# Optimization experiments

Hardware: AMD Instinct MI355X
Metric: run time of the kernel (lower is better)

Reference implementation:

```python
import jax, jax.numpy as jnp
import numpy as np

V = 512      # visible_size (channel_size, reverse_nodes=False)
H = 512      # hidden_size
FULL = V + H # full_size = 1024
T = 128      # timesteps
LAM = 0.5    # params['lambda']


def _build_lambda():
    # Lambda: (V, FULL); first V cols = lambda, hidden cols = 1, diagonal = 1
    Lam = jnp.concatenate([jnp.full((V, V), LAM, jnp.float32),
                           jnp.ones((V, H), jnp.float32)], axis=1)
    idx = jnp.arange(V)
    return Lam.at[idx, idx].set(1.0)


def setup_inputs() -> dict:
    key = jax.random.key(0)
    k1, k2, k3 = jax.random.split(key, 3)
    X = jax.random.normal(k1, (T, V), jnp.float32)
    W = jax.random.normal(k2, (FULL, FULL), jnp.float32) / np.float32(np.sqrt(FULL))
    b = jax.random.normal(k3, (FULL,), jnp.float32) * 0.01
    return {"X": X, "W": W, "b": b}


def reference(X, W, b):
    Lam = _build_lambda()          # (V, FULL)
    one_minus = 1.0 - Lam[:, :V]   # (V, V); zero on diagonal

    def step(carry, x_t):
        R, _ = carry
        WR = R @ W.T + b                           # Linear: (V, FULL)
        U = Lam * WR                               # masked recurrent part
        # Y has x_t broadcast across rows in first V cols, zeros elsewhere
        U = U.at[:, :V].add(one_minus * x_t[None, :])
        return (jax.nn.relu(U), U), None           # R = phi(U)

    init = (jnp.zeros((V, FULL), jnp.float32), jnp.zeros((V, FULL), jnp.float32))
    (_, U_last), _ = jax.lax.scan(step, init, X)
    return jnp.diagonal(U_last[:, :V])             # (V,)
```

## Files before the change

kernel.cpp:

```cpp
#include <hip/hip_runtime.h>
#include <stdint.h>

#define Vv 512
#define Ff 1024

typedef unsigned short u16;
typedef unsigned long long u64;
typedef __attribute__((ext_vector_type(8))) short s16x8;
typedef __attribute__((ext_vector_type(4))) float f32x4;

#define OFF_WH  (0ull)
#define OFF_WM  (2ull << 20)
#define OFF_WL  (4ull << 20)
#define OFF_A0  (6ull << 20)
#define OFF_A1  (9ull << 20)
#define OFF_FLG (12ull << 20)


__device__ __forceinline__ void split3(float v, u16& h, u16& m, u16& l) {
    unsigned u = __float_as_uint(v);
    float fh = __uint_as_float(u & 0xFFFF0000u);
    h = (u16)(u >> 16);
    float r1 = v - fh;
    unsigned u1 = __float_as_uint(r1);
    float fm = __uint_as_float(u1 & 0xFFFF0000u);
    m = (u16)(u1 >> 16);
    float r2 = r1 - fm;
    l = (u16)(__float_as_uint(r2) >> 16);
}

__device__ __forceinline__ float bf2f(short v) {
    return __uint_as_float(((unsigned)(u16)v) << 16);
}

__global__ void wsplit_kernel(const float* __restrict__ W, char* __restrict__ ws) {
    int idx = blockIdx.x * 256 + threadIdx.x;
    int j = idx >> 7, ko = idx & 127;
    const float* wr = W + (size_t)j * Ff + ko * 8;
    s16x8 vh, vm, vl;
#pragma unroll
    for (int e = 0; e < 8; ++e) {
        u16 h, m, l; split3(wr[e], h, m, l);
        vh[e] = (short)h; vm[e] = (short)m; vl[e] = (short)l;
    }
    int js = j >> 6, nq = (j >> 4) & 3, col = j & 15;
    int c = ko >> 3, kh = (ko >> 2) & 1, o = ko & 3;
    unsigned uhm = (unsigned)((((js * 4 + nq) * 16 + c) * 2 + kh) * 64 + o * 16 + col);
    unsigned ul  = (unsigned)(js * 8192 + (c * 2 + kh) * 256 + o * 64 + nq * 16 + col);
    *(s16x8*)(ws + OFF_WH + (size_t)uhm * 16) = vh;
    *(s16x8*)(ws + OFF_WM + (size_t)uhm * 16) = vm;
    *(s16x8*)(ws + OFF_WL + (size_t)ul * 16)  = vl;
}

__global__ void init_kernel(const float* __restrict__ X, const float* __restrict__ b,
                            char* __restrict__ ws) {
    int idx = blockIdx.x * 256 + threadIdx.x;
    if (idx < 256) ((unsigned*)(ws + OFF_FLG))[idx] = 0u;
    int i = idx >> 7, jo = idx & 127;
    s16x8 vh, vm, vl;
#pragma unroll
    for (int e = 0; e < 8; ++e) {
        int j = jo * 8 + e;
        float u = b[j];
        if (j < Vv && i != j) u = 0.5f * u + 0.5f * X[j];
        u = fmaxf(u, 0.f);
        u16 h, m, l; split3(u, h, m, l);
        vh[e] = (short)h; vm[e] = (short)m; vl[e] = (short)l;
    }
    int ig = i >> 5, r = i & 31, js = jo >> 3, o = jo & 7;
    size_t tb = (size_t)(ig * 16 + js) * 12288 + (size_t)(o * 32 + r) * 16;
    *(s16x8*)(ws + OFF_A0 + tb)        = vh;
    *(s16x8*)(ws + OFF_A0 + tb + 4096) = vm;
    *(s16x8*)(ws + OFF_A0 + tb + 8192) = vl;
}

#define GST(addr, val) \
    asm volatile("global_store_dwordx2 %0, %1, off sc0 sc1" \
                 :: "v"((void*)(addr)), "v"(val) : "memory")
#define MM(acc_, a_, b_) \
    asm("v_mfma_f32_16x16x32_bf16 %0, %1, %2, %0" : "+v"(acc_) : "v"(a_), "v"(b_))

__global__ __launch_bounds__(512, 2)
void mega_kernel(const float* __restrict__ X, const float* __restrict__ b,
                 char* __restrict__ ws) {
    extern __shared__ char smem[];
    const int tid = threadIdx.x, bid = blockIdx.x;
    const int ig = bid >> 4, js = bid & 15;
    const int lane = tid & 63, l15 = lane & 15, l4 = lane >> 4;
    const int w = tid >> 6, kh = w & 1, nq = w >> 1;

    unsigned* flg = (unsigned*)(ws + OFF_FLG);

    {
        const char* src = ws + OFF_WL + (size_t)js * 131072;
#pragma unroll
        for (int q = 0; q < 16; ++q) {
            unsigned u = (unsigned)(q * 512 + tid) * 16u;
            __builtin_amdgcn_global_load_lds(
                (const __attribute__((address_space(1))) void*)(src + u),
                (__attribute__((address_space(3))) void*)(smem + u), 16, 0, 0);
        }
    }

    s16x8 Bh0, Bh1, Bh2, Bh3, Bh4, Bh5, Bh6, Bh7, Bh8, Bh9, Bh10, Bh11, Bh12, Bh13, Bh14, Bh15;
    s16x8 Bm0, Bm1, Bm2, Bm3, Bm4, Bm5, Bm6, Bm7, Bm8, Bm9, Bm10, Bm11, Bm12, Bm13, Bm14, Bm15;
    {
        const char* wbase = ws + OFF_WH +
            (size_t)(((((js * 4 + nq) * 16) * 2 + kh) * 64) + l4 * 16 + l15) * 16;
#define LOADW(c) do {                                                                  \
        asm volatile("global_load_dwordx4 %0, %1, off"                                 \
                     : "=v"(Bh##c) : "v"((const void*)(wbase + (c) * 2048)));          \
        asm volatile("global_load_dwordx4 %0, %1, off"                                 \
                     : "=v"(Bm##c) : "v"((const void*)(wbase + (c) * 2048 + (2ull << 20)))); \
    } while (0)
        LOADW(0);  LOADW(1);  LOADW(2);  LOADW(3);
        LOADW(4);  LOADW(5);  LOADW(6);  LOADW(7);
        LOADW(8);  LOADW(9);  LOADW(10); LOADW(11);
        LOADW(12); LOADW(13); LOADW(14); LOADW(15);
#undef LOADW
    }
    asm volatile("s_waitcnt vmcnt(0)" ::: "memory");

    const int row = tid >> 4, c4 = (tid & 15) * 4;
    const int i_glob = ig * 32 + row;
    const float4 bbv = *(const float4*)(b + js * 64 + c4);
    float* red = (float*)(smem + 131072);

    const unsigned abase = (unsigned)(((kh * 4 + l4) * 32 + l15) * 16);
    const unsigned a00 = abase,          a01 = abase + 256;
    const unsigned a10 = abase + 4096,   a11 = abase + 4096 + 256;
    const unsigned a20 = abase + 8192,   a21 = abase + 8192 + 256;
    const unsigned bloff = (unsigned)(kh * 4096 + (l4 * 64 + nq * 16 + l15) * 16);

    __syncthreads();

    s16x8 Af00, Af01, Af10, Af11, Af20, Af21, Bl;
    u64 ga0, ga1, ga2, gb0, gb1, gb2;

#define GLDA3(g0_, g1_, g2_, cc) do {                                                  \
        const char* ap_ = tb + (size_t)((cc) * 12288) + (size_t)tid * 8;               \
        asm volatile("global_load_dwordx2 %0, %1, off sc0 sc1"                         \
                     : "=v"(g0_) : "v"((const void*)ap_) : "memory");                  \
        asm volatile("global_load_dwordx2 %0, %1, off sc0 sc1"                         \
                     : "=v"(g1_) : "v"((const void*)(ap_ + 4096)) : "memory");         \
        asm volatile("global_load_dwordx2 %0, %1, off sc0 sc1"                         \
                     : "=v"(g2_) : "v"((const void*)(ap_ + 8192)) : "memory");         \
    } while (0)
#define DSWR3(slot, g0_, g1_, g2_) do {                                                \
        char* wp_ = smem + 131072 + (slot) * 12288 + (size_t)tid * 8;                  \
        *(u64*)(wp_) = g0_; *(u64*)(wp_ + 4096) = g1_; *(u64*)(wp_ + 8192) = g2_;      \
    } while (0)
#define DSRD7(slot, cc) do {                                                           \
        const char* sb_ = smem + 131072 + (slot) * 12288;                              \
        Af00 = *(const s16x8*)(sb_ + a00); Af01 = *(const s16x8*)(sb_ + a01);          \
        Af10 = *(const s16x8*)(sb_ + a10); Af11 = *(const s16x8*)(sb_ + a11);          \
        Af20 = *(const s16x8*)(sb_ + a20); Af21 = *(const s16x8*)(sb_ + a21);          \
        Bl = *(const s16x8*)(smem + (cc) * 8192 + bloff);                              \
    } while (0)
#define MFMA12(c) do {                                                                 \
        __builtin_amdgcn_s_setprio(1);                                                 \
        MM(acc0, Af00, Bh##c); MM(acc1, Af01, Bh##c);                                  \
        MM(acc0, Af00, Bm##c); MM(acc1, Af01, Bm##c);                                  \
        MM(acc0, Af10, Bh##c); MM(acc1, Af11, Bh##c);                                  \
        MM(acc0, Af00, Bl);    MM(acc1, Af01, Bl);                                     \
        MM(acc0, Af20, Bh##c); MM(acc1, Af21, Bh##c);                                  \
        MM(acc0, Af10, Bm##c); MM(acc1, Af11, Bm##c);                                  \
        __builtin_amdgcn_s_setprio(0);                                                 \
    } while (0)
#define CHUNK_MID(c, P0, P1, P2, Q0, Q1, Q2) do {                                      \
        GLDA3(P0, P1, P2, (c) + 2);                                                    \
        __builtin_amdgcn_sched_barrier(0);                                             \
        MFMA12(c);                                                                     \
        __builtin_amdgcn_sched_barrier(0);                                             \
        asm volatile("s_waitcnt vmcnt(3)" ::: "memory");                               \
        DSWR3(((c) + 1) & 1, Q0, Q1, Q2);                                              \
        asm volatile("s_waitcnt lgkmcnt(0)" ::: "memory");                             \
        __builtin_amdgcn_s_barrier();                                                  \
        DSRD7(((c) + 1) & 1, (c) + 1);                                                 \
    } while (0)

    for (int t = 1; t <= 126; ++t) {
        char* srcA = ws + ((t & 1) ? OFF_A0 : OFF_A1);
        char* dstA = ws + ((t & 1) ? OFF_A1 : OFF_A0);

        if (tid < 16) {
            while ((int)__hip_atomic_load(&flg[ig * 16 + tid], __ATOMIC_RELAXED,
                                          __HIP_MEMORY_SCOPE_AGENT) < t - 1)
                __builtin_amdgcn_s_sleep(1);
        }
        __syncthreads();
        asm volatile("" ::: "memory");

        const char* tb = srcA + (size_t)ig * 16 * 12288;
        GLDA3(ga0, ga1, ga2, 0);
        GLDA3(gb0, gb1, gb2, 1);
        asm volatile("s_waitcnt vmcnt(3)" ::: "memory");
        DSWR3(0, ga0, ga1, ga2);
        asm volatile("s_waitcnt lgkmcnt(0)" ::: "memory");
        __builtin_amdgcn_s_barrier();
        DSRD7(0, 0);

        f32x4 acc0 = (f32x4){0.f, 0.f, 0.f, 0.f};
        f32x4 acc1 = (f32x4){0.f, 0.f, 0.f, 0.f};

        CHUNK_MID(0,  ga0, ga1, ga2, gb0, gb1, gb2);
        CHUNK_MID(1,  gb0, gb1, gb2, ga0, ga1, ga2);
        CHUNK_MID(2,  ga0, ga1, ga2, gb0, gb1, gb2);
        CHUNK_MID(3,  gb0, gb1, gb2, ga0, ga1, ga2);
        CHUNK_MID(4,  ga0, ga1, ga2, gb0, gb1, gb2);
        CHUNK_MID(5,  gb0, gb1, gb2, ga0, ga1, ga2);
        CHUNK_MID(6,  ga0, ga1, ga2, gb0, gb1, gb2);
        CHUNK_MID(7,  gb0, gb1, gb2, ga0, ga1, ga2);
        CHUNK_MID(8,  ga0, ga1, ga2, gb0, gb1, gb2);
        CHUNK_MID(9,  gb0, gb1, gb2, ga0, ga1, ga2);
        CHUNK_MID(10, ga0, ga1, ga2, gb0, gb1, gb2);
        CHUNK_MID(11, gb0, gb1, gb2, ga0, ga1, ga2);
        CHUNK_MID(12, ga0, ga1, ga2, gb0, gb1, gb2);
        CHUNK_MID(13, gb0, gb1, gb2, ga0, ga1, ga2);
        MFMA12(14);
        asm volatile("s_waitcnt vmcnt(0)" ::: "memory");
        DSWR3(1, gb0, gb1, gb2);
        asm volatile("s_waitcnt lgkmcnt(0)" ::: "memory");
        __builtin_amdgcn_s_barrier();
        DSRD7(1, 15);
        MFMA12(15);

        __builtin_amdgcn_s_barrier();
        asm volatile("s_nop 7\n\ts_nop 7");

#pragma unroll
        for (int r = 0; r < 4; ++r)
            red[w * 512 + (l4 * 4 + r) * 16 + l15] = acc0[r];
#pragma unroll
        for (int r = 0; r < 4; ++r)
            red[w * 512 + (16 + l4 * 4 + r) * 16 + l15] = acc1[r];
        __syncthreads();

        {
            const int nqo = c4 >> 4, cl0 = c4 & 15;
            float4 p0 = *(const float4*)&red[(nqo * 2 + 0) * 512 + row * 16 + cl0];
            float4 p1 = *(const float4*)&red[(nqo * 2 + 1) * 512 + row * 16 + cl0];
            float s0 = p0.x + p1.x, s1 = p0.y + p1.y, s2 = p0.z + p1.z, s3 = p0.w + p1.w;
            const float* xt = X + (size_t)t * Vv;
            float u0 = s0 + bbv.x, u1 = s1 + bbv.y, u2 = s2 + bbv.z, u3 = s3 + bbv.w;
            if (js < 8) {
                int j0 = js * 64 + c4;
                float x0 = xt[j0], x1 = xt[j0 + 1], x2 = xt[j0 + 2], x3 = xt[j0 + 3];
                if (i_glob != j0)     u0 = 0.5f * u0 + 0.5f * x0;
                if (i_glob != j0 + 1) u1 = 0.5f * u1 + 0.5f * x1;
                if (i_glob != j0 + 2) u2 = 0.5f * u2 + 0.5f * x2;
                if (i_glob != j0 + 3) u3 = 0.5f * u3 + 0.5f * x3;
            }
            u0 = fmaxf(u0, 0.f); u1 = fmaxf(u1, 0.f);
            u2 = fmaxf(u2, 0.f); u3 = fmaxf(u3, 0.f);
            u16 h0, m0, l0, h1, m1, l1, h2, m2, l2, h3, m3, l3;
            split3(u0, h0, m0, l0); split3(u1, h1, m1, l1);
            split3(u2, h2, m2, l2); split3(u3, h3, m3, l3);
            u64 ph = (u64)h0 | ((u64)h1 << 16) | ((u64)h2 << 32) | ((u64)h3 << 48);
            u64 pm = (u64)m0 | ((u64)m1 << 16) | ((u64)m2 << 32) | ((u64)m3 << 48);
            u64 pl = (u64)l0 | ((u64)l1 << 16) | ((u64)l2 << 32) | ((u64)l3 << 48);
            size_t tbo = (size_t)(ig * 16 + js) * 12288
                       + (size_t)((c4 >> 3) * 32 + row) * 16 + (c4 & 7) * 2;
            GST(dstA + tbo, ph);
            GST(dstA + tbo + 4096, pm);
            GST(dstA + tbo + 8192, pl);
        }
        asm volatile("s_waitcnt vmcnt(0)" ::: "memory");
        __syncthreads();
        if (tid == 0)
            __hip_atomic_store(&flg[ig * 16 + js], (unsigned)t, __ATOMIC_RELAXED,
                               __HIP_MEMORY_SCOPE_AGENT);
    }
#undef GLDA3
#undef DSWR3
#undef DSRD7
#undef MFMA12
#undef CHUNK_MID
}

__global__ void diag_kernel(const char* __restrict__ ws, const float* __restrict__ W,
                            const float* __restrict__ b, float* __restrict__ out) {
    int i = blockIdx.x, lane = threadIdx.x;
    const char* A0 = ws + OFF_A0;
    float s = 0.f;
#pragma unroll
    for (int rep = 0; rep < 2; ++rep) {
        int ko = lane + rep * 64;
        int js = ko >> 3, o = ko & 7;
        size_t tb = (size_t)((i >> 5) * 16 + js) * 12288
                  + (size_t)(o * 32 + (i & 31)) * 16;
        s16x8 vh = *(const s16x8*)(A0 + tb);
        s16x8 vm = *(const s16x8*)(A0 + tb + 4096);
        s16x8 vl = *(const s16x8*)(A0 + tb + 8192);
        const float* wr = W + (size_t)i * Ff + ko * 8;
#pragma unroll
        for (int e = 0; e < 8; ++e)
            s += (bf2f(vh[e]) + bf2f(vm[e]) + bf2f(vl[e])) * wr[e];
    }
#pragma unroll
    for (int off = 32; off > 0; off >>= 1) s += __shfl_down(s, off);
    if (lane == 0) out[i] = s + b[i];
}

extern "C" void kernel_launch(void* const* d_in, const int* in_sizes, int n_in,
                              void* d_out, int out_size, void* d_ws, size_t ws_size,
                              hipStream_t stream) {
    const float* X = (const float*)d_in[0];
    const float* W = (const float*)d_in[1];
    const float* b = (const float*)d_in[2];
    float* out = (float*)d_out;
    char* ws = (char*)d_ws;

    hipFuncSetAttribute(reinterpret_cast<const void*>(mega_kernel),
                        hipFuncAttributeMaxDynamicSharedMemorySize, 155648);

    wsplit_kernel<<<512, 256, 0, stream>>>(W, ws);
    init_kernel<<<256, 256, 0, stream>>>(X, b, ws);
    mega_kernel<<<256, 512, 155648, stream>>>(X, b, ws);
    diag_kernel<<<512, 64, 0, stream>>>(ws, W, b, out);
}
```

Baseline: 1.093 ms.

## Stream W hi/mid fragments per chunk instead of pinning them in registers

```diff
diff --git a/kernel.cpp b/kernel.cpp
--- a/kernel.cpp
+++ b/kernel.cpp
@@ -55,7 +55,7 @@
 __global__ void init_kernel(const float* __restrict__ X, const float* __restrict__ b,
                             char* __restrict__ ws) {
     int idx = blockIdx.x * 256 + threadIdx.x;
-    if (idx < 256) ((unsigned*)(ws + OFF_FLG))[idx] = 0u;
+    if (idx < 4096) ((unsigned*)(ws + OFF_FLG))[idx] = 0u;
     int i = idx >> 7, jo = idx & 127;
     s16x8 vh, vm, vl;
 #pragma unroll
@@ -102,24 +102,8 @@
         }
     }
 
-    s16x8 Bh0, Bh1, Bh2, Bh3, Bh4, Bh5, Bh6, Bh7, Bh8, Bh9, Bh10, Bh11, Bh12, Bh13, Bh14, Bh15;
-    s16x8 Bm0, Bm1, Bm2, Bm3, Bm4, Bm5, Bm6, Bm7, Bm8, Bm9, Bm10, Bm11, Bm12, Bm13, Bm14, Bm15;
-    {
-        const char* wbase = ws + OFF_WH +
-            (size_t)(((((js * 4 + nq) * 16) * 2 + kh) * 64) + l4 * 16 + l15) * 16;
-#define LOADW(c) do {                                                                  \
-        asm volatile("global_load_dwordx4 %0, %1, off"                                 \
-                     : "=v"(Bh##c) : "v"((const void*)(wbase + (c) * 2048)));          \
-        asm volatile("global_load_dwordx4 %0, %1, off"                                 \
-                     : "=v"(Bm##c) : "v"((const void*)(wbase + (c) * 2048 + (2ull << 20)))); \
-    } while (0)
-        LOADW(0);  LOADW(1);  LOADW(2);  LOADW(3);
-        LOADW(4);  LOADW(5);  LOADW(6);  LOADW(7);
-        LOADW(8);  LOADW(9);  LOADW(10); LOADW(11);
-        LOADW(12); LOADW(13); LOADW(14); LOADW(15);
-#undef LOADW
-    }
-    asm volatile("s_waitcnt vmcnt(0)" ::: "memory");
+    const char* wfrag = ws + OFF_WH +
+        (size_t)(((((js * 4 + nq) * 16) * 2 + kh) * 64) + l4 * 16 + l15) * 16;
 
     const int row = tid >> 4, c4 = (tid & 15) * 4;
     const int i_glob = ig * 32 + row;
@@ -135,8 +119,16 @@
     __syncthreads();
 
     s16x8 Af00, Af01, Af10, Af11, Af20, Af21, Bl;
+    s16x8 Wha, Wma, Whb, Wmb;
     u64 ga0, ga1, ga2, gb0, gb1, gb2;
 
+#define GLDW(H_, M_, cc) do {                                                          \
+        const char* wp_ = wfrag + (size_t)((cc) * 2048);                               \
+        asm volatile("global_load_dwordx4 %0, %1, off"                                 \
+                     : "=v"(H_) : "v"((const void*)wp_));                              \
+        asm volatile("global_load_dwordx4 %0, %1, off"                                 \
+                     : "=v"(M_) : "v"((const void*)(wp_ + (2ull << 20))));             \
+    } while (0)
 #define GLDA3(g0_, g1_, g2_, cc) do {                                                  \
         const char* ap_ = tb + (size_t)((cc) * 12288) + (size_t)tid * 8;               \
         asm volatile("global_load_dwordx2 %0, %1, off sc0 sc1"                         \
@@ -157,20 +149,21 @@
         Af20 = *(const s16x8*)(sb_ + a20); Af21 = *(const s16x8*)(sb_ + a21);          \
         Bl = *(const s16x8*)(smem + (cc) * 8192 + bloff);                              \
     } while (0)
-#define MFMA12(c) do {                                                                 \
+#define MFMA12W(H_, M_) do {                                                           \
         __builtin_amdgcn_s_setprio(1);                                                 \
-        MM(acc0, Af00, Bh##c); MM(acc1, Af01, Bh##c);                                  \
-        MM(acc0, Af00, Bm##c); MM(acc1, Af01, Bm##c);                                  \
-        MM(acc0, Af10, Bh##c); MM(acc1, Af11, Bh##c);                                  \
-        MM(acc0, Af00, Bl);    MM(acc1, Af01, Bl);                                     \
-        MM(acc0, Af20, Bh##c); MM(acc1, Af21, Bh##c);                                  \
-        MM(acc0, Af10, Bm##c); MM(acc1, Af11, Bm##c);                                  \
+        MM(acc0, Af00, H_); MM(acc1, Af01, H_);                                        \
+        MM(acc0, Af00, M_); MM(acc1, Af01, M_);                                        \
+        MM(acc0, Af10, H_); MM(acc1, Af11, H_);                                        \
+        MM(acc0, Af00, Bl); MM(acc1, Af01, Bl);                                        \
+        MM(acc0, Af20, H_); MM(acc1, Af21, H_);                                        \
+        MM(acc0, Af10, M_); MM(acc1, Af11, M_);                                        \
         __builtin_amdgcn_s_setprio(0);                                                 \
     } while (0)
-#define CHUNK_MID(c, P0, P1, P2, Q0, Q1, Q2) do {                                      \
+#define CHUNK_MID(c, P0, P1, P2, Q0, Q1, Q2, Hc, Mc, Hn, Mn) do {                      \
+        GLDW(Hn, Mn, (c) + 1);                                                         \
         GLDA3(P0, P1, P2, (c) + 2);                                                    \
         __builtin_amdgcn_sched_barrier(0);                                             \
-        MFMA12(c);                                                                     \
+        MFMA12W(Hc, Mc);                                                               \
         __builtin_amdgcn_sched_barrier(0);                                             \
         asm volatile("s_waitcnt vmcnt(3)" ::: "memory");                               \
         DSWR3(((c) + 1) & 1, Q0, Q1, Q2);                                              \
@@ -184,7 +177,7 @@
         char* dstA = ws + ((t & 1) ? OFF_A1 : OFF_A0);
 
         if (tid < 16) {
-            while ((int)__hip_atomic_load(&flg[ig * 16 + tid], __ATOMIC_RELAXED,
+            while ((int)__hip_atomic_load(&flg[(ig * 16 + tid) * 16], __ATOMIC_RELAXED,
                                           __HIP_MEMORY_SCOPE_AGENT) < t - 1)
                 __builtin_amdgcn_s_sleep(1);
         }
@@ -192,6 +185,7 @@
         asm volatile("" ::: "memory");
 
         const char* tb = srcA + (size_t)ig * 16 * 12288;
+        GLDW(Wha, Wma, 0);
         GLDA3(ga0, ga1, ga2, 0);
         GLDA3(gb0, gb1, gb2, 1);
         asm volatile("s_waitcnt vmcnt(3)" ::: "memory");
@@ -203,27 +197,28 @@
         f32x4 acc0 = (f32x4){0.f, 0.f, 0.f, 0.f};
         f32x4 acc1 = (f32x4){0.f, 0.f, 0.f, 0.f};
 
-        CHUNK_MID(0,  ga0, ga1, ga2, gb0, gb1, gb2);
-        CHUNK_MID(1,  gb0, gb1, gb2, ga0, ga1, ga2);
-        CHUNK_MID(2,  ga0, ga1, ga2, gb0, gb1, gb2);
-        CHUNK_MID(3,  gb0, gb1, gb2, ga0, ga1, ga2);
-        CHUNK_MID(4,  ga0, ga1, ga2, gb0, gb1, gb2);
-        CHUNK_MID(5,  gb0, gb1, gb2, ga0, ga1, ga2);
-        CHUNK_MID(6,  ga0, ga1, ga2, gb0, gb1, gb2);
-        CHUNK_MID(7,  gb0, gb1, gb2, ga0, ga1, ga2);
-        CHUNK_MID(8,  ga0, ga1, ga2, gb0, gb1, gb2);
-        CHUNK_MID(9,  gb0, gb1, gb2, ga0, ga1, ga2);
-        CHUNK_MID(10, ga0, ga1, ga2, gb0, gb1, gb2);
-        CHUNK_MID(11, gb0, gb1, gb2, ga0, ga1, ga2);
-        CHUNK_MID(12, ga0, ga1, ga2, gb0, gb1, gb2);
-        CHUNK_MID(13, gb0, gb1, gb2, ga0, ga1, ga2);
-        MFMA12(14);
+        CHUNK_MID(0,  ga0, ga1, ga2, gb0, gb1, gb2, Wha, Wma, Whb, Wmb);
+        CHUNK_MID(1,  gb0, gb1, gb2, ga0, ga1, ga2, Whb, Wmb, Wha, Wma);
+        CHUNK_MID(2,  ga0, ga1, ga2, gb0, gb1, gb2, Wha, Wma, Whb, Wmb);
+        CHUNK_MID(3,  gb0, gb1, gb2, ga0, ga1, ga2, Whb, Wmb, Wha, Wma);
+        CHUNK_MID(4,  ga0, ga1, ga2, gb0, gb1, gb2, Wha, Wma, Whb, Wmb);
+        CHUNK_MID(5,  gb0, gb1, gb2, ga0, ga1, ga2, Whb, Wmb, Wha, Wma);
+        CHUNK_MID(6,  ga0, ga1, ga2, gb0, gb1, gb2, Wha, Wma, Whb, Wmb);
+        CHUNK_MID(7,  gb0, gb1, gb2, ga0, ga1, ga2, Whb, Wmb, Wha, Wma);
+        CHUNK_MID(8,  ga0, ga1, ga2, gb0, gb1, gb2, Wha, Wma, Whb, Wmb);
+        CHUNK_MID(9,  gb0, gb1, gb2, ga0, ga1, ga2, Whb, Wmb, Wha, Wma);
+        CHUNK_MID(10, ga0, ga1, ga2, gb0, gb1, gb2, Wha, Wma, Whb, Wmb);
+        CHUNK_MID(11, gb0, gb1, gb2, ga0, ga1, ga2, Whb, Wmb, Wha, Wma);
+        CHUNK_MID(12, ga0, ga1, ga2, gb0, gb1, gb2, Wha, Wma, Whb, Wmb);
+        CHUNK_MID(13, gb0, gb1, gb2, ga0, ga1, ga2, Whb, Wmb, Wha, Wma);
+        GLDW(Whb, Wmb, 15);
+        MFMA12W(Wha, Wma);
         asm volatile("s_waitcnt vmcnt(0)" ::: "memory");
         DSWR3(1, gb0, gb1, gb2);
         asm volatile("s_waitcnt lgkmcnt(0)" ::: "memory");
         __builtin_amdgcn_s_barrier();
         DSRD7(1, 15);
-        MFMA12(15);
+        MFMA12W(Whb, Wmb);
 
         __builtin_amdgcn_s_barrier();
         asm volatile("s_nop 7\n\ts_nop 7");
@@ -268,13 +263,14 @@
         asm volatile("s_waitcnt vmcnt(0)" ::: "memory");
         __syncthreads();
         if (tid == 0)
-            __hip_atomic_store(&flg[ig * 16 + js], (unsigned)t, __ATOMIC_RELAXED,
+            __hip_atomic_store(&flg[(ig * 16 + js) * 16], (unsigned)t, __ATOMIC_RELAXED,
                                __HIP_MEMORY_SCOPE_AGENT);
     }
+#undef GLDW
 #undef GLDA3
 #undef DSWR3
 #undef DSRD7
-#undef MFMA12
+#undef MFMA12W
 #undef CHUNK_MID
 }
 
```

New measurement: 1.457 ms. 33.2% more time.

## Start each block on its own K-chunk, pad flags, deepen A prefetch

Applied to the files above, without the earlier changes.

```diff
diff --git a/kernel.cpp b/kernel.cpp
--- a/kernel.cpp
+++ b/kernel.cpp
@@ -55,7 +55,7 @@
 __global__ void init_kernel(const float* __restrict__ X, const float* __restrict__ b,
                             char* __restrict__ ws) {
     int idx = blockIdx.x * 256 + threadIdx.x;
-    if (idx < 256) ((unsigned*)(ws + OFF_FLG))[idx] = 0u;
+    if (idx < 4096) ((unsigned*)(ws + OFF_FLG))[idx] = 0u;
     int i = idx >> 7, jo = idx & 127;
     s16x8 vh, vm, vl;
 #pragma unroll
@@ -105,13 +105,14 @@
     s16x8 Bh0, Bh1, Bh2, Bh3, Bh4, Bh5, Bh6, Bh7, Bh8, Bh9, Bh10, Bh11, Bh12, Bh13, Bh14, Bh15;
     s16x8 Bm0, Bm1, Bm2, Bm3, Bm4, Bm5, Bm6, Bm7, Bm8, Bm9, Bm10, Bm11, Bm12, Bm13, Bm14, Bm15;
     {
-        const char* wbase = ws + OFF_WH +
+        const char* wfrag = ws + OFF_WH +
             (size_t)(((((js * 4 + nq) * 16) * 2 + kh) * 64) + l4 * 16 + l15) * 16;
-#define LOADW(c) do {                                                                  \
+#define LOADW(n) do {                                                                  \
+        const char* wp_ = wfrag + (size_t)(((js + (n)) & 15) * 2048);                  \
         asm volatile("global_load_dwordx4 %0, %1, off"                                 \
-                     : "=v"(Bh##c) : "v"((const void*)(wbase + (c) * 2048)));          \
+                     : "=v"(Bh##n) : "v"((const void*)wp_));                           \
         asm volatile("global_load_dwordx4 %0, %1, off"                                 \
-                     : "=v"(Bm##c) : "v"((const void*)(wbase + (c) * 2048 + (2ull << 20)))); \
+                     : "=v"(Bm##n) : "v"((const void*)(wp_ + (2ull << 20))));          \
     } while (0)
         LOADW(0);  LOADW(1);  LOADW(2);  LOADW(3);
         LOADW(4);  LOADW(5);  LOADW(6);  LOADW(7);
@@ -119,12 +120,12 @@
         LOADW(12); LOADW(13); LOADW(14); LOADW(15);
 #undef LOADW
     }
-    asm volatile("s_waitcnt vmcnt(0)" ::: "memory");
 
     const int row = tid >> 4, c4 = (tid & 15) * 4;
     const int i_glob = ig * 32 + row;
     const float4 bbv = *(const float4*)(b + js * 64 + c4);
     float* red = (float*)(smem + 131072);
+    const unsigned ownoff = (unsigned)(((c4 >> 3) * 32 + row) * 16 + (c4 & 7) * 2);
 
     const unsigned abase = (unsigned)(((kh * 4 + l4) * 32 + l15) * 16);
     const unsigned a00 = abase,          a01 = abase + 256;
@@ -132,10 +133,8 @@
     const unsigned a20 = abase + 8192,   a21 = abase + 8192 + 256;
     const unsigned bloff = (unsigned)(kh * 4096 + (l4 * 64 + nq * 16 + l15) * 16);
 
-    __syncthreads();
-
     s16x8 Af00, Af01, Af10, Af11, Af20, Af21, Bl;
-    u64 ga0, ga1, ga2, gb0, gb1, gb2;
+    u64 ga0, ga1, ga2, gb0, gb1, gb2, gc0, gc1, gc2;
 
 #define GLDA3(g0_, g1_, g2_, cc) do {                                                  \
         const char* ap_ = tb + (size_t)((cc) * 12288) + (size_t)tid * 8;               \
@@ -155,74 +154,86 @@
         Af00 = *(const s16x8*)(sb_ + a00); Af01 = *(const s16x8*)(sb_ + a01);          \
         Af10 = *(const s16x8*)(sb_ + a10); Af11 = *(const s16x8*)(sb_ + a11);          \
         Af20 = *(const s16x8*)(sb_ + a20); Af21 = *(const s16x8*)(sb_ + a21);          \
-        Bl = *(const s16x8*)(smem + (cc) * 8192 + bloff);                              \
-    } while (0)
-#define MFMA12(c) do {                                                                 \
+        Bl = *(const s16x8*)(smem + (size_t)((cc) * 8192) + bloff);                    \
+    } while (0)
+#define MFMA12(n) do {                                                                 \
         __builtin_amdgcn_s_setprio(1);                                                 \
-        MM(acc0, Af00, Bh##c); MM(acc1, Af01, Bh##c);                                  \
-        MM(acc0, Af00, Bm##c); MM(acc1, Af01, Bm##c);                                  \
-        MM(acc0, Af10, Bh##c); MM(acc1, Af11, Bh##c);                                  \
+        MM(acc0, Af00, Bh##n); MM(acc1, Af01, Bh##n);                                  \
+        MM(acc0, Af00, Bm##n); MM(acc1, Af01, Bm##n);                                  \
+        MM(acc0, Af10, Bh##n); MM(acc1, Af11, Bh##n);                                  \
         MM(acc0, Af00, Bl);    MM(acc1, Af01, Bl);                                     \
-        MM(acc0, Af20, Bh##c); MM(acc1, Af21, Bh##c);                                  \
-        MM(acc0, Af10, Bm##c); MM(acc1, Af11, Bm##c);                                  \
+        MM(acc0, Af20, Bh##n); MM(acc1, Af21, Bh##n);                                  \
+        MM(acc0, Af10, Bm##n); MM(acc1, Af11, Bm##n);                                  \
         __builtin_amdgcn_s_setprio(0);                                                 \
     } while (0)
-#define CHUNK_MID(c, P0, P1, P2, Q0, Q1, Q2) do {                                      \
-        GLDA3(P0, P1, P2, (c) + 2);                                                    \
+#define CHUNK(n, P0, P1, P2, Q0, Q1, Q2, VM) do {                                      \
         __builtin_amdgcn_sched_barrier(0);                                             \
-        MFMA12(c);                                                                     \
+        MFMA12(n);                                                                     \
         __builtin_amdgcn_sched_barrier(0);                                             \
-        asm volatile("s_waitcnt vmcnt(3)" ::: "memory");                               \
-        DSWR3(((c) + 1) & 1, Q0, Q1, Q2);                                              \
+        asm volatile("s_waitcnt vmcnt(" #VM ")" ::: "memory");                         \
+        DSWR3(((n) + 1) & 1, Q0, Q1, Q2);                                              \
         asm volatile("s_waitcnt lgkmcnt(0)" ::: "memory");                             \
         __builtin_amdgcn_s_barrier();                                                  \
-        DSRD7(((c) + 1) & 1, (c) + 1);                                                 \
-    } while (0)
+        DSRD7(((n) + 1) & 1, (js + (n) + 1) & 15);                                     \
+    } while (0)
+
+    {
+        const char* own0 = ws + OFF_A0 + (size_t)(ig * 16 + js) * 12288;
+        const char* tb = own0;
+        GLDA3(ga0, ga1, ga2, 0);
+        asm volatile("s_waitcnt vmcnt(0)" ::: "memory");
+        DSWR3(0, ga0, ga1, ga2);
+    }
+    __syncthreads();
 
     for (int t = 1; t <= 126; ++t) {
         char* srcA = ws + ((t & 1) ? OFF_A0 : OFF_A1);
         char* dstA = ws + ((t & 1) ? OFF_A1 : OFF_A0);
-
-        if (tid < 16) {
-            while ((int)__hip_atomic_load(&flg[ig * 16 + tid], __ATOMIC_RELAXED,
+        const char* tb = srcA + (size_t)ig * 16 * 12288;
+
+        DSRD7(0, js);
+
+        if (lane < 16) {
+            while ((int)__hip_atomic_load(&flg[(ig * 16 + lane) * 16], __ATOMIC_RELAXED,
                                           __HIP_MEMORY_SCOPE_AGENT) < t - 1)
                 __builtin_amdgcn_s_sleep(1);
         }
-        __syncthreads();
         asm volatile("" ::: "memory");
 
-        const char* tb = srcA + (size_t)ig * 16 * 12288;
-        GLDA3(ga0, ga1, ga2, 0);
-        GLDA3(gb0, gb1, gb2, 1);
-        asm volatile("s_waitcnt vmcnt(3)" ::: "memory");
-        DSWR3(0, ga0, ga1, ga2);
-        asm volatile("s_waitcnt lgkmcnt(0)" ::: "memory");
-        __builtin_amdgcn_s_barrier();
-        DSRD7(0, 0);
+        GLDA3(gb0, gb1, gb2, (js + 1) & 15);
+        GLDA3(gc0, gc1, gc2, (js + 2) & 15);
 
         f32x4 acc0 = (f32x4){0.f, 0.f, 0.f, 0.f};
         f32x4 acc1 = (f32x4){0.f, 0.f, 0.f, 0.f};
 
-        CHUNK_MID(0,  ga0, ga1, ga2, gb0, gb1, gb2);
-        CHUNK_MID(1,  gb0, gb1, gb2, ga0, ga1, ga2);
-        CHUNK_MID(2,  ga0, ga1, ga2, gb0, gb1, gb2);
-        CHUNK_MID(3,  gb0, gb1, gb2, ga0, ga1, ga2);
-        CHUNK_MID(4,  ga0, ga1, ga2, gb0, gb1, gb2);
-        CHUNK_MID(5,  gb0, gb1, gb2, ga0, ga1, ga2);
-        CHUNK_MID(6,  ga0, ga1, ga2, gb0, gb1, gb2);
-        CHUNK_MID(7,  gb0, gb1, gb2, ga0, ga1, ga2);
-        CHUNK_MID(8,  ga0, ga1, ga2, gb0, gb1, gb2);
-        CHUNK_MID(9,  gb0, gb1, gb2, ga0, ga1, ga2);
-        CHUNK_MID(10, ga0, ga1, ga2, gb0, gb1, gb2);
-        CHUNK_MID(11, gb0, gb1, gb2, ga0, ga1, ga2);
-        CHUNK_MID(12, ga0, ga1, ga2, gb0, gb1, gb2);
-        CHUNK_MID(13, gb0, gb1, gb2, ga0, ga1, ga2);
-        MFMA12(14);
-        asm volatile("s_waitcnt vmcnt(0)" ::: "memory");
-        DSWR3(1, gb0, gb1, gb2);
-        asm volatile("s_waitcnt lgkmcnt(0)" ::: "memory");
-        __builtin_amdgcn_s_barrier();
-        DSRD7(1, 15);
+        GLDA3(ga0, ga1, ga2, (js + 3) & 15);
+        CHUNK(0,  ga0, ga1, ga2, gb0, gb1, gb2, 6);
+        GLDA3(gb0, gb1, gb2, (js + 4) & 15);
+        CHUNK(1,  gb0, gb1, gb2, gc0, gc1, gc2, 6);
+        GLDA3(gc0, gc1, gc2, (js + 5) & 15);
+        CHUNK(2,  gc0, gc1, gc2, ga0, ga1, ga2, 6);
+        GLDA3(ga0, ga1, ga2, (js + 6) & 15);
+        CHUNK(3,  ga0, ga1, ga2, gb0, gb1, gb2, 6);
+        GLDA3(gb0, gb1, gb2, (js + 7) & 15);
+        CHUNK(4,  gb0, gb1, gb2, gc0, gc1, gc2, 6);
+        GLDA3(gc0, gc1, gc2, (js + 8) & 15);
+        CHUNK(5,  gc0, gc1, gc2, ga0, ga1, ga2, 6);
+        GLDA3(ga0, ga1, ga2, (js + 9) & 15);
+        CHUNK(6,  ga0, ga1, ga2, gb0, gb1, gb2, 6);
+        GLDA3(gb0, gb1, gb2, (js + 10) & 15);
+        CHUNK(7,  gb0, gb1, gb2, gc0, gc1, gc2, 6);
+        GLDA3(gc0, gc1, gc2, (js + 11) & 15);
+        CHUNK(8,  gc0, gc1, gc2, ga0, ga1, ga2, 6);
+        GLDA3(ga0, ga1, ga2, (js + 12) & 15);
+        CHUNK(9,  ga0, ga1, ga2, gb0, gb1, gb2, 6);
+        GLDA3(gb0, gb1, gb2, (js + 13) & 15);
+        CHUNK(10, gb0, gb1, gb2, gc0, gc1, gc2, 6);
+        GLDA3(gc0, gc1, gc2, (js + 14) & 15);
+        CHUNK(11, gc0, gc1, gc2, ga0, ga1, ga2, 6);
+        GLDA3(ga0, ga1, ga2, (js + 15) & 15);
+        CHUNK(12, ga0, ga1, ga2, gb0, gb1, gb2, 6);
+        CHUNK(13, ga0, ga1, ga2, gc0, gc1, gc2, 3);
+        CHUNK(14, ga0, ga1, ga2, ga0, ga1, ga2, 0);
         MFMA12(15);
 
         __builtin_amdgcn_s_barrier();
@@ -236,10 +247,12 @@
             red[w * 512 + (16 + l4 * 4 + r) * 16 + l15] = acc1[r];
         __syncthreads();
 
+        const int nqo = c4 >> 4, cl0 = c4 & 15;
+        float4 p0 = *(const float4*)&red[(nqo * 2 + 0) * 512 + row * 16 + cl0];
+        float4 p1 = *(const float4*)&red[(nqo * 2 + 1) * 512 + row * 16 + cl0];
+        __syncthreads();
+
         {
-            const int nqo = c4 >> 4, cl0 = c4 & 15;
-            float4 p0 = *(const float4*)&red[(nqo * 2 + 0) * 512 + row * 16 + cl0];
-            float4 p1 = *(const float4*)&red[(nqo * 2 + 1) * 512 + row * 16 + cl0];
             float s0 = p0.x + p1.x, s1 = p0.y + p1.y, s2 = p0.z + p1.z, s3 = p0.w + p1.w;
             const float* xt = X + (size_t)t * Vv;
             float u0 = s0 + bbv.x, u1 = s1 + bbv.y, u2 = s2 + bbv.z, u3 = s3 + bbv.w;
@@ -259,23 +272,25 @@
             u64 ph = (u64)h0 | ((u64)h1 << 16) | ((u64)h2 << 32) | ((u64)h3 << 48);
             u64 pm = (u64)m0 | ((u64)m1 << 16) | ((u64)m2 << 32) | ((u64)m3 << 48);
             u64 pl = (u64)l0 | ((u64)l1 << 16) | ((u64)l2 << 32) | ((u64)l3 << 48);
-            size_t tbo = (size_t)(ig * 16 + js) * 12288
-                       + (size_t)((c4 >> 3) * 32 + row) * 16 + (c4 & 7) * 2;
+            size_t tbo = (size_t)(ig * 16 + js) * 12288 + ownoff;
             GST(dstA + tbo, ph);
             GST(dstA + tbo + 4096, pm);
             GST(dstA + tbo + 8192, pl);
+            *(u64*)(smem + 131072 + ownoff) = ph;
+            *(u64*)(smem + 131072 + ownoff + 4096) = pm;
+            *(u64*)(smem + 131072 + ownoff + 8192) = pl;
         }
         asm volatile("s_waitcnt vmcnt(0)" ::: "memory");
         __syncthreads();
         if (tid == 0)
-            __hip_atomic_store(&flg[ig * 16 + js], (unsigned)t, __ATOMIC_RELAXED,
+            __hip_atomic_store(&flg[(ig * 16 + js) * 16], (unsigned)t, __ATOMIC_RELAXED,
                                __HIP_MEMORY_SCOPE_AGENT);
     }
 #undef GLDA3
 #undef DSWR3
 #undef DSRD7
 #undef MFMA12
-#undef CHUNK_MID
+#undef CHUNK
 }
 
 __global__ void diag_kernel(const char* __restrict__ ws, const float* __restrict__ W,
```

New measurement: 932.1 us, median of 2. -14.7%, faster.
